# Performance work log

Measured on AMD Instinct MI355X. Metric: run time of the kernel, lower is better.

Reference implementation:

```python
import jax, jax.numpy as jnp
import numpy as np

THRESH = 0.5
BETA = 0.25


def setup_inputs() -> dict:
    key = jax.random.key(0)
    # [T, B, C, H, W] time-major spiking CNN activations
    x = jax.random.normal(key, (8, 32, 128, 32, 32), dtype=jnp.float32)
    return {"x": x}


def reference(x) -> jnp.ndarray:
    """Leaky integrate-and-fire scan over the leading time axis.

    mem[t] = beta * mem[t-1] + x[t]
    s[t]   = heaviside(mem[t] - thresh)
    mem[t] <- mem[t] * (1 - s[t])   # hard reset after spike
    Returns spikes with the same shape as x.
    """

    def step(mem, xt):
        mem = mem * BETA + xt
        spk = (mem >= THRESH).astype(xt.dtype)
        mem = mem * (1.0 - spk)  # hard reset
        return mem, spk

    mem0 = jnp.zeros_like(x[0])
    _, spikes = jax.lax.scan(step, mem0, x)
    return spikes
```

## Files before the change

kernel.cpp:

```cpp
#include <hip/hip_runtime.h>


#define LIF_THRESH 0.5f
#define LIF_BETA   0.25f
#define LIF_T      8

typedef float v4f __attribute__((ext_vector_type(4)));

__device__ __forceinline__ float lif_step(float& m, float xv) {
    m = m * LIF_BETA + xv;
    float s = (m >= LIF_THRESH) ? 1.f : 0.f;
    m = (m >= LIF_THRESH) ? 0.f : m;
    return s;
}

__global__ __launch_bounds__(256) void lif_kernel(const v4f* __restrict__ x,
                                                  v4f* __restrict__ out,
                                                  int n4, int half) {
    int tid = blockIdx.x * 256 + threadIdx.x;
    if (tid >= half) return;
    const int ia = tid;
    const int ib = tid + half;

    v4f xa[LIF_T], xb[LIF_T];
#pragma unroll
    for (int t = 0; t < LIF_T; ++t) xa[t] = x[(size_t)t * n4 + ia];
#pragma unroll
    for (int t = 0; t < LIF_T; ++t) xb[t] = x[(size_t)t * n4 + ib];
    __builtin_amdgcn_sched_barrier(0);

    float ma0 = 0.f, ma1 = 0.f, ma2 = 0.f, ma3 = 0.f;
    float mb0 = 0.f, mb1 = 0.f, mb2 = 0.f, mb3 = 0.f;
#pragma unroll
    for (int t = 0; t < LIF_T; ++t) {
        v4f sa, sb;
        sa.x = lif_step(ma0, xa[t].x);
        sa.y = lif_step(ma1, xa[t].y);
        sa.z = lif_step(ma2, xa[t].z);
        sa.w = lif_step(ma3, xa[t].w);
        sb.x = lif_step(mb0, xb[t].x);
        sb.y = lif_step(mb1, xb[t].y);
        sb.z = lif_step(mb2, xb[t].z);
        sb.w = lif_step(mb3, xb[t].w);
        __builtin_nontemporal_store(sa, &out[(size_t)t * n4 + ia]);
        __builtin_nontemporal_store(sb, &out[(size_t)t * n4 + ib]);
    }
}

extern "C" void kernel_launch(void* const* d_in, const int* in_sizes, int n_in,
                              void* d_out, int out_size, void* d_ws, size_t ws_size,
                              hipStream_t stream) {
    const v4f* x = (const v4f*)d_in[0];
    v4f* out = (v4f*)d_out;

    long long total = in_sizes[0];
    int n = (int)(total / LIF_T);
    int n4 = n / 4;
    int half = n4 / 2;

    dim3 block(256);
    dim3 grid((half + 255) / 256);
    lif_kernel<<<grid, block, 0, stream>>>(x, out, n4, half);
}
```

Measured before the change: 241.7 us.

## Software-pipeline LIF loads with inline asm and four columns per thread

```diff
diff --git a/kernel.cpp b/kernel.cpp
--- a/kernel.cpp
+++ b/kernel.cpp
@@ -4,6 +4,8 @@
 #define LIF_THRESH 0.5f
 #define LIF_BETA   0.25f
 #define LIF_T      8
+#define BLOCK      256
+#define JITER      4
 
 typedef float v4f __attribute__((ext_vector_type(4)));
 
@@ -14,37 +16,91 @@
     return s;
 }
 
-__global__ __launch_bounds__(256) void lif_kernel(const v4f* __restrict__ x,
-                                                  v4f* __restrict__ out,
-                                                  int n4, int half) {
-    int tid = blockIdx.x * 256 + threadIdx.x;
-    if (tid >= half) return;
-    const int ia = tid;
-    const int ib = tid + half;
+#define ISSUE8(r0, r1, r2, r3, r4, r5, r6, r7, COL)                                            \
+    {                                                                                          \
+        const v4f* _p = x + (size_t)(COL);                                                     \
+        asm volatile("global_load_dwordx4 %0, %1, off" : "=v"(r0) : "v"(_p) : "memory");       \
+        _p += n4;                                                                              \
+        asm volatile("global_load_dwordx4 %0, %1, off" : "=v"(r1) : "v"(_p) : "memory");       \
+        _p += n4;                                                                              \
+        asm volatile("global_load_dwordx4 %0, %1, off" : "=v"(r2) : "v"(_p) : "memory");       \
+        _p += n4;                                                                              \
+        asm volatile("global_load_dwordx4 %0, %1, off" : "=v"(r3) : "v"(_p) : "memory");       \
+        _p += n4;                                                                              \
+        asm volatile("global_load_dwordx4 %0, %1, off" : "=v"(r4) : "v"(_p) : "memory");       \
+        _p += n4;                                                                              \
+        asm volatile("global_load_dwordx4 %0, %1, off" : "=v"(r5) : "v"(_p) : "memory");       \
+        _p += n4;                                                                              \
+        asm volatile("global_load_dwordx4 %0, %1, off" : "=v"(r6) : "v"(_p) : "memory");       \
+        _p += n4;                                                                              \
+        asm volatile("global_load_dwordx4 %0, %1, off" : "=v"(r7) : "v"(_p) : "memory");       \
+    }
 
-    v4f xa[LIF_T], xb[LIF_T];
-#pragma unroll
-    for (int t = 0; t < LIF_T; ++t) xa[t] = x[(size_t)t * n4 + ia];
-#pragma unroll
-    for (int t = 0; t < LIF_T; ++t) xb[t] = x[(size_t)t * n4 + ib];
-    __builtin_amdgcn_sched_barrier(0);
+#define WAIT8(r0, r1, r2, r3, r4, r5, r6, r7, CNT)                                             \
+    asm volatile("s_waitcnt vmcnt(" #CNT ")"                                                   \
+                 : "+v"(r0), "+v"(r1), "+v"(r2), "+v"(r3),                                     \
+                   "+v"(r4), "+v"(r5), "+v"(r6), "+v"(r7)                                      \
+                 :                                                                             \
+                 : "memory");
 
-    float ma0 = 0.f, ma1 = 0.f, ma2 = 0.f, ma3 = 0.f;
-    float mb0 = 0.f, mb1 = 0.f, mb2 = 0.f, mb3 = 0.f;
-#pragma unroll
-    for (int t = 0; t < LIF_T; ++t) {
-        v4f sa, sb;
-        sa.x = lif_step(ma0, xa[t].x);
-        sa.y = lif_step(ma1, xa[t].y);
-        sa.z = lif_step(ma2, xa[t].z);
-        sa.w = lif_step(ma3, xa[t].w);
-        sb.x = lif_step(mb0, xb[t].x);
-        sb.y = lif_step(mb1, xb[t].y);
-        sb.z = lif_step(mb2, xb[t].z);
-        sb.w = lif_step(mb3, xb[t].w);
-        __builtin_nontemporal_store(sa, &out[(size_t)t * n4 + ia]);
-        __builtin_nontemporal_store(sb, &out[(size_t)t * n4 + ib]);
+#define COMPUTE_STORE(r0, r1, r2, r3, r4, r5, r6, r7, COL)                                     \
+    {                                                                                          \
+        float m0 = 0.f, m1 = 0.f, m2 = 0.f, m3 = 0.f;                                          \
+        v4f s;                                                                                 \
+        v4f* _q = out + (size_t)(COL);                                                         \
+        s.x = lif_step(m0, r0.x); s.y = lif_step(m1, r0.y);                                    \
+        s.z = lif_step(m2, r0.z); s.w = lif_step(m3, r0.w);                                    \
+        __builtin_nontemporal_store(s, _q); _q += n4;                                          \
+        s.x = lif_step(m0, r1.x); s.y = lif_step(m1, r1.y);                                    \
+        s.z = lif_step(m2, r1.z); s.w = lif_step(m3, r1.w);                                    \
+        __builtin_nontemporal_store(s, _q); _q += n4;                                          \
+        s.x = lif_step(m0, r2.x); s.y = lif_step(m1, r2.y);                                    \
+        s.z = lif_step(m2, r2.z); s.w = lif_step(m3, r2.w);                                    \
+        __builtin_nontemporal_store(s, _q); _q += n4;                                          \
+        s.x = lif_step(m0, r3.x); s.y = lif_step(m1, r3.y);                                    \
+        s.z = lif_step(m2, r3.z); s.w = lif_step(m3, r3.w);                                    \
+        __builtin_nontemporal_store(s, _q); _q += n4;                                          \
+        s.x = lif_step(m0, r4.x); s.y = lif_step(m1, r4.y);                                    \
+        s.z = lif_step(m2, r4.z); s.w = lif_step(m3, r4.w);                                    \
+        __builtin_nontemporal_store(s, _q); _q += n4;                                          \
+        s.x = lif_step(m0, r5.x); s.y = lif_step(m1, r5.y);                                    \
+        s.z = lif_step(m2, r5.z); s.w = lif_step(m3, r5.w);                                    \
+        __builtin_nontemporal_store(s, _q); _q += n4;                                          \
+        s.x = lif_step(m0, r6.x); s.y = lif_step(m1, r6.y);                                    \
+        s.z = lif_step(m2, r6.z); s.w = lif_step(m3, r6.w);                                    \
+        __builtin_nontemporal_store(s, _q); _q += n4;                                          \
+        s.x = lif_step(m0, r7.x); s.y = lif_step(m1, r7.y);                                    \
+        s.z = lif_step(m2, r7.z); s.w = lif_step(m3, r7.w);                                    \
+        __builtin_nontemporal_store(s, _q);                                                    \
     }
+
+__global__ __launch_bounds__(BLOCK, 1) void lif_kernel(const v4f* __restrict__ x,
+                                                       v4f* __restrict__ out,
+                                                       int n4) {
+    const int c0 = blockIdx.x * (BLOCK * JITER) + threadIdx.x;
+    const int c1 = c0 + BLOCK;
+    const int c2 = c1 + BLOCK;
+    const int c3 = c2 + BLOCK;
+
+    v4f a0, a1, a2, a3, a4, a5, a6, a7;
+    v4f b0, b1, b2, b3, b4, b5, b6, b7;
+
+    ISSUE8(a0, a1, a2, a3, a4, a5, a6, a7, c0)
+    ISSUE8(b0, b1, b2, b3, b4, b5, b6, b7, c1)
+
+    WAIT8(a0, a1, a2, a3, a4, a5, a6, a7, 8)
+    COMPUTE_STORE(a0, a1, a2, a3, a4, a5, a6, a7, c0)
+    ISSUE8(a0, a1, a2, a3, a4, a5, a6, a7, c2)
+
+    WAIT8(b0, b1, b2, b3, b4, b5, b6, b7, 16)
+    COMPUTE_STORE(b0, b1, b2, b3, b4, b5, b6, b7, c1)
+    ISSUE8(b0, b1, b2, b3, b4, b5, b6, b7, c3)
+
+    WAIT8(a0, a1, a2, a3, a4, a5, a6, a7, 16)
+    COMPUTE_STORE(a0, a1, a2, a3, a4, a5, a6, a7, c2)
+
+    WAIT8(b0, b1, b2, b3, b4, b5, b6, b7, 8)
+    COMPUTE_STORE(b0, b1, b2, b3, b4, b5, b6, b7, c3)
 }
 
 extern "C" void kernel_launch(void* const* d_in, const int* in_sizes, int n_in,
@@ -56,9 +112,8 @@
     long long total = in_sizes[0];
     int n = (int)(total / LIF_T);
     int n4 = n / 4;
-    int half = n4 / 2;
 
-    dim3 block(256);
-    dim3 grid((half + 255) / 256);
-    lif_kernel<<<grid, block, 0, stream>>>(x, out, n4, half);
+    dim3 block(BLOCK);
+    dim3 grid(n4 / (BLOCK * JITER));
+    lif_kernel<<<grid, block, 0, stream>>>(x, out, n4);
 }
```

Result: no change. 241.1 us (-0.2%).
